# Kernel tuning notes

Hardware: AMD Instinct MI355X
Metric: run time of the kernel (lower is better)

## Reference

```python
import jax, jax.numpy as jnp
import numpy as np

B, C, N, H = 4, 512, 2048, 8
D = C // H  # per-head depth = 64
EPS = 1e-5


def conv1x1(x, W, b):
    # x: [B, Cin, N], W: [Cout, Cin], b: [Cout]
    return jnp.einsum('oc,bcn->bon', W, x) + b[None, :, None]


def instance_norm(x):
    # normalize over length dim per (batch, channel), no affine
    mu = jnp.mean(x, axis=-1, keepdims=True)
    var = jnp.var(x, axis=-1, keepdims=True)
    return (x - mu) * jax.lax.rsqrt(var + EPS)


def _pipeline(src, tgt, Wq, bq, Wk, bk, Wv, bv, Wm, bm):
    # query from src, key/value from tgt; reshape C -> (D outer, H inner)
    q = conv1x1(src, Wq, bq).reshape(B, D, H, N)
    k = conv1x1(tgt, Wk, bk).reshape(B, D, H, N)
    v = conv1x1(tgt, Wv, bv).reshape(B, D, H, N)
    scores = jnp.einsum('bdhn,bdhm->bhnm', q, k) / jnp.sqrt(jnp.float32(D))
    probs = jax.nn.softmax(scores, axis=-1)
    out = jnp.einsum('bhnm,bdhm->bdhn', probs, v).reshape(B, C, N)
    return conv1x1(out, Wm, bm)


def _mlp(x, W1, b1, W2, b2):
    h = conv1x1(x, W1, b1)
    h = jax.nn.relu(instance_norm(h))
    return conv1x1(h, W2, b2)


def setup_inputs() -> dict:
    key = jax.random.key(0)
    ks = jax.random.split(key, 8)
    s = 0.02
    return {
        'source_features': jax.random.normal(ks[0], (B, C, N), jnp.float32),
        'target_features': jax.random.normal(ks[1], (B, C, N), jnp.float32),
        'Wq': jax.random.normal(ks[2], (C, C), jnp.float32) * s,
        'bq': jnp.zeros((C,), jnp.float32),
        'Wk': jax.random.normal(ks[3], (C, C), jnp.float32) * s,
        'bk': jnp.zeros((C,), jnp.float32),
        'Wv': jax.random.normal(ks[4], (C, C), jnp.float32) * s,
        'bv': jnp.zeros((C,), jnp.float32),
        'Wm': jax.random.normal(ks[5], (C, C), jnp.float32) * s,
        'bm': jnp.zeros((C,), jnp.float32),
        'W1': jax.random.normal(ks[6], (2 * C, 2 * C), jnp.float32) * s,
        'b1': jnp.zeros((2 * C,), jnp.float32),
        'W2': jax.random.normal(ks[7], (C, 2 * C), jnp.float32) * s,
        'b2': jnp.zeros((C,), jnp.float32),
    }


def reference(source_features, target_features, Wq, bq, Wk, bk, Wv, bv, Wm, bm, W1, b1, W2, b2):
    src, tgt = source_features, target_features
    # source update uses ORIGINAL target features
    src_att = _pipeline(src, tgt, Wq, bq, Wk, bk, Wv, bv, Wm, bm)
    src = src + _mlp(jnp.concatenate([src, src_att], axis=1), W1, b1, W2, b2)
    # target update uses the UPDATED source features (in-place semantics of original)
    tgt_att = _pipeline(tgt, src, Wq, bq, Wk, bk, Wv, bv, Wm, bm)
    tgt = tgt + _mlp(jnp.concatenate([tgt, tgt_att], axis=1), W1, b1, W2, b2)
    return src, tgt
```

## Files before the change

### kernel.cpp

```cpp
#include <hip/hip_runtime.h>

#define NN 2048
#define CC 512
#define BB 4
#define HH 8
#define DD 64
#define SCALE 0.18033688011112043f

typedef unsigned short u16;
typedef __attribute__((ext_vector_type(8))) short bf16x8;
typedef __attribute__((ext_vector_type(4))) float f32x4;

extern "C" __device__ float __ocml_native_exp2_f32(float);

__device__ inline u16 f2b(float x) {
    unsigned u = __builtin_bit_cast(unsigned, x);
    u += 0x7fffu + ((u >> 16) & 1u);
    return (u16)(u >> 16);
}
__device__ inline float b2f(u16 h) {
    unsigned u = ((unsigned)h) << 16;
    return __builtin_bit_cast(float, u);
}

#define GLD16(g, l) __builtin_amdgcn_global_load_lds( \
    (const __attribute__((address_space(1))) unsigned int*)(g), \
    (__attribute__((address_space(3))) unsigned int*)(l), 16, 0, 0)

template<int JT, bool DBUF>
__device__ __forceinline__ void gemm_core_t(
    const u16* __restrict__ Xa, const u16* __restrict__ Xb, int Ca, int K,
    const u16* __restrict__ Wt, size_t rowBase,
    u16* As, u16* Bs, f32x4 (&acc)[4][JT])
{
    constexpr int OT = JT * 32;
    constexpr int ASZ = 128 * 64, BSZ = OT * 64;
    const int tid = threadIdx.x;
    const int lane = tid & 63, w = tid >> 6;
    const int quad = lane >> 4, l16 = lane & 15;
    const int wrow = w & 1, wcol = w >> 1;
    const int arow = lane >> 3, aseg = lane & 7;
    const int asw = aseg ^ arow;
    const int lk = l16 & 7;

    auto stage = [&](int k0, u16* Ad, u16* Bd) {
        const u16* Xs; int Crow, cc;
        if (k0 < Ca) { Xs = Xa; Crow = Ca; cc = k0; }
        else         { Xs = Xb; Crow = K - Ca; cc = k0 - Ca; }
#pragma unroll
        for (int i = 0; i < 4; ++i) {
            int rl = w * 32 + i * 8 + arow;
            int la = __builtin_amdgcn_readfirstlane((w * 32 + i * 8) * 64);
            GLD16(Xs + (rowBase + rl) * (size_t)Crow + cc + asw * 8, (char*)Ad + (size_t)la * 2);
        }
#pragma unroll
        for (int i = 0; i < OT / 32; ++i) {
            int rl = w * (OT / 4) + i * 8 + arow;
            int la = __builtin_amdgcn_readfirstlane((w * (OT / 4) + i * 8) * 64);
            GLD16(Wt + (size_t)rl * K + k0 + asw * 8, (char*)Bd + (size_t)la * 2);
        }
    };
    auto compute = [&](const u16* Ac, const u16* Bc) {
#pragma unroll
        for (int kk = 0; kk < 2; ++kk) {
            const int g = ((kk * 4 + quad) ^ lk) * 8;
            bf16x8 av[4], bv[JT];
#pragma unroll
            for (int i = 0; i < 4; ++i)
                av[i] = *(const bf16x8*)&Ac[(wrow * 64 + i * 16 + l16) * 64 + g];
#pragma unroll
            for (int jj = 0; jj < JT; ++jj)
                bv[jj] = *(const bf16x8*)&Bc[(wcol * JT * 16 + jj * 16 + l16) * 64 + g];
#pragma unroll
            for (int i = 0; i < 4; ++i)
#pragma unroll
                for (int jj = 0; jj < JT; ++jj)
                    acc[i][jj] = __builtin_amdgcn_mfma_f32_16x16x32_bf16(av[i], bv[jj], acc[i][jj], 0, 0, 0);
        }
    };

    if constexpr (DBUF) {
        stage(0, As, Bs);
        const int nt = K / 64;
        for (int t = 0; t < nt; ++t) {
            const u16* Ac = As + (t & 1) * ASZ;
            const u16* Bc = Bs + (t & 1) * BSZ;
            __syncthreads();
            if (t + 1 < nt)
                stage((t + 1) * 64, As + ((t + 1) & 1) * ASZ, Bs + ((t + 1) & 1) * BSZ);
            compute(Ac, Bc);
        }
    } else {
        for (int k0 = 0; k0 < K; k0 += 64) {
            stage(k0, As, Bs);
            __syncthreads();
            compute(As, Bs);
            __syncthreads();
        }
    }
}

template<int JT>
__device__ __forceinline__ void gemm_epilogue_t(
    f32x4 (&acc)[4][JT], const float* __restrict__ bias, int mode,
    int b, int n0, int o0, int Cout,
    const float* __restrict__ res, float* __restrict__ outF, u16* __restrict__ outB)
{
    const int tid = threadIdx.x;
    const int lane = tid & 63, w = tid >> 6;
    const int quad = lane >> 4, l16 = lane & 15;
    const int wrow = w & 1, wcol = w >> 1;
    const size_t bN = (size_t)b * NN;
    const int nb0 = n0 + wrow * 64, ob0 = o0 + wcol * JT * 16;

    if (mode == 0) {
#pragma unroll
        for (int j = 0; j < JT; ++j) {
            int o = ob0 + j * 16 + l16;
            float bs = bias[o];
#pragma unroll
            for (int i = 0; i < 4; ++i)
#pragma unroll
                for (int r = 0; r < 4; ++r) {
                    int n = nb0 + i * 16 + quad * 4 + r;
                    outB[(bN + n) * Cout + o] = f2b(acc[i][j][r] + bs);
                }
        }
    } else if (mode == 1) {
#pragma unroll
        for (int j = 0; j < JT; ++j) {
            int o = ob0 + j * 16 + l16;
            float bs = bias[o];
            int h = o >> 6, d = o & 63;
#pragma unroll
            for (int i = 0; i < 4; ++i) {
                int n = nb0 + i * 16 + quad * 4;
                ushort4 pk;
                pk.x = f2b(acc[i][j][0] + bs); pk.y = f2b(acc[i][j][1] + bs);
                pk.z = f2b(acc[i][j][2] + bs); pk.w = f2b(acc[i][j][3] + bs);
                *(ushort4*)&outB[(((size_t)b * HH + h) * DD + d) * NN + n] = pk;
            }
        }
    } else {
#pragma unroll
        for (int j = 0; j < JT; ++j) {
            int o = ob0 + j * 16 + l16;
            float bs = bias[o];
#pragma unroll
            for (int i = 0; i < 4; ++i) {
                int n = nb0 + i * 16 + quad * 4;
                size_t ad = ((size_t)b * Cout + o) * NN + n;
                float4 rv = *(const float4*)&res[ad];
                float4 yv;
                yv.x = acc[i][j][0] + bs + rv.x;
                yv.y = acc[i][j][1] + bs + rv.y;
                yv.z = acc[i][j][2] + bs + rv.z;
                yv.w = acc[i][j][3] + bs + rv.w;
                *(float4*)&outF[ad] = yv;
                if (mode == 2) {
                    outB[(bN + n + 0) * Cout + o] = f2b(yv.x);
                    outB[(bN + n + 1) * Cout + o] = f2b(yv.y);
                    outB[(bN + n + 2) * Cout + o] = f2b(yv.z);
                    outB[(bN + n + 3) * Cout + o] = f2b(yv.w);
                }
            }
        }
    }
}

template<int JT>
__global__ __launch_bounds__(256, 3) void gemm_bf16_t(
    const u16* __restrict__ Wb, const float* __restrict__ bias,
    const u16* __restrict__ Xa, const u16* __restrict__ Xb,
    int Ca, int K, int Cout,
    const float* __restrict__ res, float* __restrict__ outF,
    u16* __restrict__ outB, int mode)
{
    __shared__ u16 As[2 * 128 * 64];
    __shared__ u16 Bs[2 * JT * 32 * 64];
    const int b = blockIdx.z, n0 = blockIdx.x * 128, o0 = blockIdx.y * (JT * 32);
    f32x4 acc[4][JT] = {};
    gemm_core_t<JT, true>(Xa, Xb, Ca, K, Wb + (size_t)o0 * K, (size_t)b * NN + n0, As, Bs, acc);
    gemm_epilogue_t<JT>(acc, bias, mode, b, n0, o0, Cout, res, outF, outB);
}

template<bool DBUF>
__device__ __forceinline__ void gemm_core8(
    const u16* __restrict__ Xa, const u16* __restrict__ Xb, int Ca, int K,
    const u16* __restrict__ Wt, size_t rowBase,
    u16* As, u16* Bs, f32x4 (&acc)[4][2])
{
    constexpr int ASZ = 128 * 64, BSZ = 128 * 64;
    const int tid = threadIdx.x;
    const int lane = tid & 63, w = tid >> 6;
    const int quad = lane >> 4, l16 = lane & 15;
    const int wr = w & 1, wc = w >> 1;
    const int arow = lane >> 3, aseg = lane & 7;
    const int asw = aseg ^ arow;
    const int lk = l16 & 7;

    auto stage = [&](int k0, u16* Ad, u16* Bd) {
        const u16* Xs; int Crow, cc;
        if (k0 < Ca) { Xs = Xa; Crow = Ca; cc = k0; }
        else         { Xs = Xb; Crow = K - Ca; cc = k0 - Ca; }
#pragma unroll
        for (int i = 0; i < 2; ++i) {
            int rl = w * 16 + i * 8 + arow;
            int la = __builtin_amdgcn_readfirstlane((w * 16 + i * 8) * 64);
            GLD16(Xs + (rowBase + rl) * (size_t)Crow + cc + asw * 8, (char*)Ad + (size_t)la * 2);
            GLD16(Wt + (size_t)rl * K + k0 + asw * 8, (char*)Bd + (size_t)la * 2);
        }
    };
    auto compute = [&](const u16* Ac, const u16* Bc) {
#pragma unroll
        for (int kk = 0; kk < 2; ++kk) {
            const int g = ((kk * 4 + quad) ^ lk) * 8;
            bf16x8 av[4], bv[2];
#pragma unroll
            for (int i = 0; i < 4; ++i)
                av[i] = *(const bf16x8*)&Ac[(wr * 64 + i * 16 + l16) * 64 + g];
#pragma unroll
            for (int j = 0; j < 2; ++j)
                bv[j] = *(const bf16x8*)&Bc[(wc * 32 + j * 16 + l16) * 64 + g];
#pragma unroll
            for (int i = 0; i < 4; ++i)
#pragma unroll
                for (int j = 0; j < 2; ++j)
                    acc[i][j] = __builtin_amdgcn_mfma_f32_16x16x32_bf16(av[i], bv[j], acc[i][j], 0, 0, 0);
        }
    };

    if constexpr (DBUF) {
        stage(0, As, Bs);
        const int nt = K / 64;
        for (int t = 0; t < nt; ++t) {
            const u16* Ac = As + (t & 1) * ASZ;
            const u16* Bc = Bs + (t & 1) * BSZ;
            __syncthreads();
            if (t + 1 < nt)
                stage((t + 1) * 64, As + ((t + 1) & 1) * ASZ, Bs + ((t + 1) & 1) * BSZ);
            compute(Ac, Bc);
        }
    } else {
        for (int k0 = 0; k0 < K; k0 += 64) {
            stage(k0, As, Bs);
            __syncthreads();
            compute(As, Bs);
            __syncthreads();
        }
    }
}

__device__ __forceinline__ void gemm_epilogue8(
    f32x4 (&acc)[4][2], const float* __restrict__ bias, int mode,
    int b, int n0, int o0, int Cout, u16* __restrict__ outB)
{
    const int tid = threadIdx.x;
    const int lane = tid & 63, w = tid >> 6;
    const int quad = lane >> 4, l16 = lane & 15;
    const int wr = w & 1, wc = w >> 1;
    const size_t bN = (size_t)b * NN;
    const int nb0 = n0 + wr * 64, ob0 = o0 + wc * 32;

    if (mode == 0) {
#pragma unroll
        for (int j = 0; j < 2; ++j) {
            int o = ob0 + j * 16 + l16;
            float bs = bias[o];
#pragma unroll
            for (int i = 0; i < 4; ++i)
#pragma unroll
                for (int r = 0; r < 4; ++r) {
                    int n = nb0 + i * 16 + quad * 4 + r;
                    outB[(bN + n) * Cout + o] = f2b(acc[i][j][r] + bs);
                }
        }
    } else {
#pragma unroll
        for (int j = 0; j < 2; ++j) {
            int o = ob0 + j * 16 + l16;
            float bs = bias[o];
            int h = o >> 6, d = o & 63;
#pragma unroll
            for (int i = 0; i < 4; ++i) {
                int n = nb0 + i * 16 + quad * 4;
                ushort4 pk;
                pk.x = f2b(acc[i][j][0] + bs); pk.y = f2b(acc[i][j][1] + bs);
                pk.z = f2b(acc[i][j][2] + bs); pk.w = f2b(acc[i][j][3] + bs);
                *(ushort4*)&outB[(((size_t)b * HH + h) * DD + d) * NN + n] = pk;
            }
        }
    }
}

__global__ __launch_bounds__(512, 4) void gemm_qkv(
    const u16* __restrict__ WQ, const float* __restrict__ bQ,
    const u16* __restrict__ XQ, u16* __restrict__ outQ,
    const u16* __restrict__ WK, const float* __restrict__ bK, u16* __restrict__ outK,
    const u16* __restrict__ WV, const float* __restrict__ bV, u16* __restrict__ outV,
    const u16* __restrict__ XKV)
{
    __shared__ u16 As[2 * 128 * 64];
    __shared__ u16 Bs[2 * 128 * 64];
    const int yb = blockIdx.y;
    const u16* W; const float* bias; const u16* X; u16* outB; int mode, o0;
    if (yb < 4)      { o0 = yb * 128;       W = WQ; bias = bQ; X = XQ;  outB = outQ; mode = 0; }
    else if (yb < 8) { o0 = (yb - 4) * 128; W = WK; bias = bK; X = XKV; outB = outK; mode = 0; }
    else             { o0 = (yb - 8) * 128; W = WV; bias = bV; X = XKV; outB = outV; mode = 1; }
    const int b = blockIdx.z, n0 = blockIdx.x * 128;
    f32x4 acc[4][2] = {};
    gemm_core8<true>(X, nullptr, 512, 512, W + (size_t)o0 * 512, (size_t)b * NN + n0, As, Bs, acc);
    gemm_epilogue8(acc, bias, mode, b, n0, o0, 512, outB);
}

__global__ __launch_bounds__(512, 4) void gemm_w1(
    const u16* __restrict__ Wb, const float* __restrict__ bias,
    const u16* __restrict__ Xa, const u16* __restrict__ Xb,
    u16* __restrict__ outB, float* __restrict__ Ssum, float* __restrict__ Ssq)
{
    __shared__ u16 As[2 * 128 * 64];
    __shared__ u16 Bs[2 * 128 * 64];
    const int b = blockIdx.z, n0 = blockIdx.x * 128, o0 = blockIdx.y * 128;
    f32x4 acc[4][2] = {};
    gemm_core8<true>(Xa, Xb, 512, 1024, Wb + (size_t)o0 * 1024, (size_t)b * NN + n0, As, Bs, acc);

    const int tid = threadIdx.x;
    const int lane = tid & 63, w = tid >> 6;
    const int quad = lane >> 4, l16 = lane & 15;
    const int wr = w & 1, wc = w >> 1;
    const size_t bN = (size_t)b * NN;
    const int nb0 = n0 + wr * 64, ob0 = o0 + wc * 32;

#pragma unroll
    for (int j = 0; j < 2; ++j) {
        int o = ob0 + j * 16 + l16;
        float bs = bias[o];
        float s = 0.f, q = 0.f;
#pragma unroll
        for (int i = 0; i < 4; ++i)
#pragma unroll
            for (int r = 0; r < 4; ++r) {
                int n = nb0 + i * 16 + quad * 4 + r;
                float y = acc[i][j][r] + bs;
                s += y; q += y * y;
                outB[(bN + n) * 1024 + o] = f2b(y);
            }
        s += __shfl_xor(s, 16); s += __shfl_xor(s, 32);
        q += __shfl_xor(q, 16); q += __shfl_xor(q, 32);
        if (quad == 0) {
            atomicAdd(&Ssum[b * 1024 + o], s);
            atomicAdd(&Ssq[b * 1024 + o], q);
        }
    }
}

__global__ __launch_bounds__(512, 4) void attn(
    const u16* __restrict__ Qg, const u16* __restrict__ Kg,
    const u16* __restrict__ Vg, u16* __restrict__ Og)
{
    __shared__ __align__(16) u16 pool[6 * 4096];
    u16* const Ksb[2] = { pool, pool + 4096 };
    u16* const Vtb[2] = { pool + 2 * 4096, pool + 3 * 4096 };
    u16* const Ps = pool + 4 * 4096;
    const int tid = threadIdx.x;
    const int lane = tid & 63, w = tid >> 6;
    const int qg = w & 3, hv = w >> 2;
    const int quad = lane >> 4, l16 = lane & 15;
    const int id = blockIdx.x;
    const int xcd = id & 7, jj = id >> 3;
    const int bh = xcd * 4 + (jj >> 4), nb = jj & 15;
    const int b = bh >> 3, h = bh & 7;
    const int n0 = nb * 128, wn0 = qg * 32;
    const int sr0 = w * 8;
    const size_t qkBase = ((size_t)b * NN) * CC + h * DD;
    const size_t vBase  = (((size_t)b * HH + h) * DD) * NN;
    const int r8 = lane >> 3, seg = lane & 7;
    const int segp = seg ^ r8;
    const int lk = l16 & 7;

    const u16* kp = Kg + qkBase + (size_t)(sr0 + r8) * CC + segp * 8;
    const u16* vp = Vg + vBase + (size_t)(sr0 + r8) * NN + segp * 8;

    bf16x8 qf[2][2];
#pragma unroll
    for (int qs = 0; qs < 2; ++qs) {
        int n = n0 + wn0 + qs * 16 + l16;
#pragma unroll
        for (int ks = 0; ks < 2; ++ks)
            qf[qs][ks] = *(const bf16x8*)&Qg[qkBase + (size_t)n * CC + ks * 32 + quad * 8];
    }

    const short oneb = 0x3F80;
    const bf16x8 ones = {oneb, oneb, oneb, oneb, oneb, oneb, oneb, oneb};
    f32x4 oa[2][4] = {};
    f32x4 lacc[2] = {};

    GLD16(kp, Ksb[0] + sr0 * 64);
    GLD16(vp, Vtb[0] + sr0 * 64);
    kp += 64 * CC; vp += 64;

#define ATTN_PREF(BUF) do { \
        GLD16(kp, Ksb[BUF] + sr0 * 64); \
        GLD16(vp, Vtb[BUF] + sr0 * 64); \
        kp += 64 * CC; vp += 64; \
    } while (0)

#define ATTN_BODY(CUR) do { \
        const u16* ksb = Ksb[CUR]; \
        const u16* vtb = Vtb[CUR]; \
        f32x4 st[2][2] = {}; \
        _Pragma("unroll") \
        for (int ks = 0; ks < 2; ++ks) { \
            bf16x8 ak[2]; \
            _Pragma("unroll") \
            for (int rtl = 0; rtl < 2; ++rtl) \
                ak[rtl] = *(const bf16x8*)&ksb[(hv * 32 + rtl * 16 + l16) * 64 + ((ks * 4 + quad) ^ lk) * 8]; \
            __builtin_amdgcn_s_setprio(1); \
            _Pragma("unroll") \
            for (int rtl = 0; rtl < 2; ++rtl) \
                _Pragma("unroll") \
                for (int qs = 0; qs < 2; ++qs) \
                    st[qs][rtl] = __builtin_amdgcn_mfma_f32_16x16x32_bf16(ak[rtl], qf[qs][ks], st[qs][rtl], 0, 0, 0); \
            __builtin_amdgcn_s_setprio(0); \
        } \
        _Pragma("unroll") \
        for (int qs = 0; qs < 2; ++qs) { \
            int nrow = wn0 + qs * 16 + l16; \
            _Pragma("unroll") \
            for (int rtl = 0; rtl < 2; ++rtl) { \
                unsigned u0 = __builtin_bit_cast(unsigned, __ocml_native_exp2_f32(st[qs][rtl][0])); \
                unsigned u1 = __builtin_bit_cast(unsigned, __ocml_native_exp2_f32(st[qs][rtl][1])); \
                unsigned u2 = __builtin_bit_cast(unsigned, __ocml_native_exp2_f32(st[qs][rtl][2])); \
                unsigned u3 = __builtin_bit_cast(unsigned, __ocml_native_exp2_f32(st[qs][rtl][3])); \
                uint2 t; \
                t.x = __builtin_amdgcn_perm(u1, u0, 0x07060302u); \
                t.y = __builtin_amdgcn_perm(u3, u2, 0x07060302u); \
                int g = (((hv * 2 + rtl) * 2 + (quad >> 1))) ^ lk; \
                *(uint2*)&Ps[nrow * 64 + g * 8 + (quad & 1) * 4] = t; \
            } \
        } \
        { \
            bf16x8 pa[2]; \
            _Pragma("unroll") \
            for (int qs = 0; qs < 2; ++qs) \
                pa[qs] = *(const bf16x8*)&Ps[(wn0 + qs * 16 + l16) * 64 + ((hv * 4 + quad) ^ lk) * 8]; \
            bf16x8 vb[4]; \
            _Pragma("unroll") \
            for (int ct = 0; ct < 4; ++ct) \
                vb[ct] = *(const bf16x8*)&vtb[(ct * 16 + l16) * 64 + ((hv * 4 + quad) ^ lk) * 8]; \
            __builtin_amdgcn_s_setprio(1); \
            _Pragma("unroll") \
            for (int ct = 0; ct < 4; ++ct) \
                _Pragma("unroll") \
                for (int qs = 0; qs < 2; ++qs) \
                    oa[qs][ct] = __builtin_amdgcn_mfma_f32_16x16x32_bf16(pa[qs], vb[ct], oa[qs][ct], 0, 0, 0); \
            _Pragma("unroll") \
            for (int qs = 0; qs < 2; ++qs) \
                lacc[qs] = __builtin_amdgcn_mfma_f32_16x16x32_bf16(pa[qs], ones, lacc[qs], 0, 0, 0); \
            __builtin_amdgcn_s_setprio(0); \
        } \
    } while (0)

    for (int it = 0; it < NN / 64; it += 2) {
        __syncthreads();
        ATTN_PREF(1);
        ATTN_BODY(0);
        __syncthreads();
        if (it < NN / 64 - 2)
            ATTN_PREF(0);
        ATTN_BODY(1);
    }
#undef ATTN_PREF
#undef ATTN_BODY

    __syncthreads();
    float* M = (float*)pool;
    const int mbase = (qg * 64 + lane) * 44;
    if (hv == 1) {
#pragma unroll
        for (int qs = 0; qs < 2; ++qs)
#pragma unroll
            for (int ct = 0; ct < 4; ++ct)
                *(f32x4*)&M[mbase + (qs * 4 + ct) * 4] = oa[qs][ct];
        *(f32x4*)&M[mbase + 32] = lacc[0];
        *(f32x4*)&M[mbase + 36] = lacc[1];
    }
    __syncthreads();
    if (hv == 0) {
#pragma unroll
        for (int qs = 0; qs < 2; ++qs)
#pragma unroll
            for (int ct = 0; ct < 4; ++ct)
                oa[qs][ct] += *(const f32x4*)&M[mbase + (qs * 4 + ct) * 4];
        lacc[0] += *(const f32x4*)&M[mbase + 32];
        lacc[1] += *(const f32x4*)&M[mbase + 36];
#pragma unroll
        for (int qs = 0; qs < 2; ++qs)
#pragma unroll
            for (int r = 0; r < 4; ++r) {
                float li = 1.f / lacc[qs][r];
                int n = n0 + wn0 + qs * 16 + quad * 4 + r;
#pragma unroll
                for (int ct = 0; ct < 4; ++ct)
                    Og[qkBase + (size_t)n * CC + ct * 16 + l16] = f2b(oa[qs][ct][r] * li);
            }
    }
}

__global__ __launch_bounds__(256) void transpose_cvt(
    const float* __restrict__ X, u16* __restrict__ Y)
{
    __shared__ float T[64][65];
    const int tid = threadIdx.x;
    const int n0 = blockIdx.x * 64, c0 = blockIdx.y * 64, b = blockIdx.z;
    const int rr = tid >> 4, cc4 = tid & 15;
#pragma unroll
    for (int p = 0; p < 4; ++p) {
        int cl = p * 16 + rr;
        float4 v = *(const float4*)&X[((size_t)b * CC + c0 + cl) * NN + n0 + cc4 * 4];
        T[cl][cc4 * 4 + 0] = v.x; T[cl][cc4 * 4 + 1] = v.y;
        T[cl][cc4 * 4 + 2] = v.z; T[cl][cc4 * 4 + 3] = v.w;
    }
    __syncthreads();
#pragma unroll
    for (int p = 0; p < 4; ++p) {
        int nl = p * 16 + rr;
        ushort4 pk;
        pk.x = f2b(T[cc4 * 4 + 0][nl]);
        pk.y = f2b(T[cc4 * 4 + 1][nl]);
        pk.z = f2b(T[cc4 * 4 + 2][nl]);
        pk.w = f2b(T[cc4 * 4 + 3][nl]);
        *(ushort4*)&Y[((size_t)b * NN + n0 + nl) * CC + c0 + cc4 * 4] = pk;
    }
}

__global__ __launch_bounds__(256) void prep_weights(
    const float* __restrict__ Wq, const float* __restrict__ Wk,
    const float* __restrict__ Wv, const float* __restrict__ Wm,
    const float* __restrict__ W1, const float* __restrict__ W2,
    u16* oQ, u16* oK, u16* oV, u16* oM, u16* o1, u16* o2)
{
    const float* W; u16* o; int rows, cols, perm; float sc = 1.f;
    switch (blockIdx.z) {
        case 0: W = Wq; o = oQ; rows = 512;  cols = 512;  perm = 1; sc = SCALE; break;
        case 1: W = Wk; o = oK; rows = 512;  cols = 512;  perm = 1; break;
        case 2: W = Wv; o = oV; rows = 512;  cols = 512;  perm = 1; break;
        case 3: W = Wm; o = oM; rows = 512;  cols = 512;  perm = 2; break;
        case 4: W = W1; o = o1; rows = 1024; cols = 1024; perm = 0; break;
        default: W = W2; o = o2; rows = 512; cols = 1024; perm = 0; break;
    }
    int c = blockIdx.x * 256 + threadIdx.x;
    int r = blockIdx.y;
    if (r >= rows || c >= cols) return;
    int sr = r, scol = c;
    if (perm == 1) sr = (r & 63) * 8 + (r >> 6);
    else if (perm == 2) scol = (c & 63) * 8 + (c >> 6);
    o[(size_t)r * cols + c] = f2b(W[(size_t)sr * cols + scol] * sc);
}

__global__ void prep_bias(const float* __restrict__ bq, const float* __restrict__ bk,
                          const float* __restrict__ bv,
                          float* oq, float* ok, float* ov)
{
    int i = blockIdx.x * 256 + threadIdx.x;
    int y = blockIdx.y;
    const float* s = (y == 0) ? bq : (y == 1) ? bk : bv;
    float* o = (y == 0) ? oq : (y == 1) ? ok : ov;
    float v = s[(i & 63) * 8 + (i >> 6)];
    if (y == 0) v *= SCALE;
    o[i] = v;
}

__global__ __launch_bounds__(256) void inorm_p2(
    u16* __restrict__ X, const float* __restrict__ Ssum, const float* __restrict__ Ssq)
{
    const int tid = threadIdx.x;
    const int cidx = (tid & 127) * 8;
    const int rq = tid >> 7;
    const int b = blockIdx.y, nz = blockIdx.x;
    float4 s0 = *(const float4*)&Ssum[b * 1024 + cidx];
    float4 s1 = *(const float4*)&Ssum[b * 1024 + cidx + 4];
    float4 q0 = *(const float4*)&Ssq[b * 1024 + cidx];
    float4 q1 = *(const float4*)&Ssq[b * 1024 + cidx + 4];
    float mean[8] = { s0.x, s0.y, s0.z, s0.w, s1.x, s1.y, s1.z, s1.w };
    float sq[8]   = { q0.x, q0.y, q0.z, q0.w, q1.x, q1.y, q1.z, q1.w };
    float rstd[8];
#pragma unroll
    for (int j = 0; j < 8; ++j) {
        float m = mean[j] * (1.f / NN);
        float v = sq[j] * (1.f / NN) - m * m;
        mean[j] = m; rstd[j] = rsqrtf(fmaxf(v, 0.f) + 1e-5f);
    }
    size_t base = ((size_t)b * NN + nz * 16 + rq * 8) * 1024 + cidx;
    for (int i = 0; i < 8; ++i) {
        bf16x8 v = *(const bf16x8*)&X[base + (size_t)i * 1024];
        bf16x8 o;
#pragma unroll
        for (int j = 0; j < 8; ++j) {
            float x = b2f((u16)v[j]);
            x = (x - mean[j]) * rstd[j];
            o[j] = (short)f2b(fmaxf(x, 0.f));
        }
        *(bf16x8*)&X[base + (size_t)i * 1024] = o;
    }
}

extern "C" void kernel_launch(void* const* d_in, const int* in_sizes, int n_in,
                              void* d_out, int out_size, void* d_ws, size_t ws_size,
                              hipStream_t stream)
{
    (void)in_sizes; (void)n_in; (void)out_size; (void)ws_size;
    const float* src = (const float*)d_in[0];
    const float* tgt = (const float*)d_in[1];
    const float* Wq = (const float*)d_in[2];  const float* bq = (const float*)d_in[3];
    const float* Wk = (const float*)d_in[4];  const float* bk = (const float*)d_in[5];
    const float* Wv = (const float*)d_in[6];  const float* bv = (const float*)d_in[7];
    const float* Wm = (const float*)d_in[8];  const float* bm = (const float*)d_in[9];
    const float* W1 = (const float*)d_in[10]; const float* b1 = (const float*)d_in[11];
    const float* W2 = (const float*)d_in[12]; const float* b2 = (const float*)d_in[13];

    char* w = (char*)d_ws;
    u16* WQp = (u16*)(w);
    u16* WKp = (u16*)(w + (512u << 10));
    u16* WVp = (u16*)(w + (1u << 20));
    u16* WMp = (u16*)(w + (3u << 19));
    u16* W1b = (u16*)(w + (2u << 20));
    u16* W2b = (u16*)(w + (4u << 20));
    float* BQp = (float*)(w + (5u << 20));
    float* BKp = BQp + 512;
    float* BVp = BQp + 1024;
    float* STS = BQp + 1536;
    float* STQ = STS + 4096;
    u16* X0 = (u16*)(w + ( 6u << 20));
    u16* X1 = (u16*)(w + (14u << 20));
    u16* B0 = (u16*)(w + (22u << 20));
    u16* B1 = (u16*)(w + (30u << 20));
    u16* B2 = (u16*)(w + (38u << 20));
    u16* B3 = (u16*)(w + (46u << 20));

    float* out = (float*)d_out;
    const size_t R = (size_t)BB * CC * NN;
    dim3 blk(256), blkA(512);

    prep_weights<<<dim3(4, 1024, 6), blk, 0, stream>>>(Wq, Wk, Wv, Wm, W1, W2,
                                                       WQp, WKp, WVp, WMp, W1b, W2b);
    prep_bias<<<dim3(2, 3), blk, 0, stream>>>(bq, bk, bv, BQp, BKp, BVp);
    transpose_cvt<<<dim3(32, 8, 4), blk, 0, stream>>>(src, X0);
    transpose_cvt<<<dim3(32, 8, 4), blk, 0, stream>>>(tgt, X1);

    dim3 gQKV(16, 12, 4), gM(16, 8, 4), gW1(16, 8, 4), gW2(16, 8, 4), gIN(128, 4);

    gemm_qkv<<<gQKV, blkA, 0, stream>>>(WQp, BQp, X0, B0, WKp, BKp, B1, WVp, BVp, B2, X1);
    attn<<<dim3(512), blkA, 0, stream>>>(B0, B1, B2, B3);
    gemm_bf16_t<2><<<gM, blk, 0, stream>>>(WMp, bm, B3, nullptr, 512, 512, 512, nullptr, nullptr, B0, 0);
    hipMemsetAsync(STS, 0, 8192 * sizeof(float), stream);
    gemm_w1<<<gW1, blkA, 0, stream>>>(W1b, b1, X0, B0, B1, STS, STQ);
    inorm_p2<<<gIN, blk, 0, stream>>>(B1, STS, STQ);
    gemm_bf16_t<2><<<gW2, blk, 0, stream>>>(W2b, b2, B1, nullptr, 1024, 1024, 512, src, out, B3, 2);

    gemm_qkv<<<gQKV, blkA, 0, stream>>>(WQp, BQp, X1, X0, WKp, BKp, B0, WVp, BVp, B1, B3);
    attn<<<dim3(512), blkA, 0, stream>>>(X0, B0, B1, B2);
    gemm_bf16_t<2><<<gM, blk, 0, stream>>>(WMp, bm, B2, nullptr, 512, 512, 512, nullptr, nullptr, X0, 0);
    hipMemsetAsync(STS, 0, 8192 * sizeof(float), stream);
    gemm_w1<<<gW1, blkA, 0, stream>>>(W1b, b1, X1, X0, B0, STS, STQ);
    inorm_p2<<<gIN, blk, 0, stream>>>(B0, STS, STQ);
    gemm_bf16_t<2><<<gW2, blk, 0, stream>>>(W2b, b2, B0, nullptr, 1024, 1024, 512, tgt, out + R, nullptr, 3);
}
```

Baseline: 384.5 us.

## Keep attention probabilities in registers, split keys across waves, use 16x16x16 MFMA for PV

The attention kernel is restructured so each 256-thread block handles 64 queries. Each of its 4 waves takes a 16-key slice of every 64-key tile. The exp'd score fragments are packed straight into bf16x4 registers and fed to a 16x16x16 bf16 MFMA for P·V. This removes the LDS round-trip for P and the extra MFMA against a ones vector that computed row sums, which are now accumulated as scalar sums. In exchange, the four waves' partial outputs must be tree-reduced through LDS with extra barriers at the end, and each block reloads K/V for fewer queries, which doubles K/V traffic.

```diff
diff --git a/kernel.cpp b/kernel.cpp
--- a/kernel.cpp
+++ b/kernel.cpp
@@ -9,9 +9,21 @@
 
 typedef unsigned short u16;
 typedef __attribute__((ext_vector_type(8))) short bf16x8;
+typedef __attribute__((ext_vector_type(4))) short bf16x4;
 typedef __attribute__((ext_vector_type(4))) float f32x4;
 
 extern "C" __device__ float __ocml_native_exp2_f32(float);
+
+#if __has_builtin(__builtin_amdgcn_mfma_f32_16x16x16bf16_1k)
+#define MFMA16(A, B, C) __builtin_amdgcn_mfma_f32_16x16x16bf16_1k(A, B, C, 0, 0, 0)
+#else
+__device__ __forceinline__ f32x4 mfma16_asm(bf16x4 a, bf16x4 b, f32x4 c) {
+    f32x4 d;
+    asm("v_mfma_f32_16x16x16_bf16 %0, %1, %2, %3" : "=v"(d) : "v"(a), "v"(b), "0"(c));
+    return d;
+}
+#define MFMA16(A, B, C) mfma16_asm(A, B, C)
+#endif
 
 __device__ inline u16 f2b(float x) {
     unsigned u = __builtin_bit_cast(unsigned, x);
@@ -354,111 +366,101 @@
     }
 }
 
-__global__ __launch_bounds__(512, 4) void attn(
+__global__ __launch_bounds__(256, 3) void attn(
     const u16* __restrict__ Qg, const u16* __restrict__ Kg,
     const u16* __restrict__ Vg, u16* __restrict__ Og)
 {
-    __shared__ __align__(16) u16 pool[6 * 4096];
+    __shared__ __align__(16) u16 pool[17664];
     u16* const Ksb[2] = { pool, pool + 4096 };
     u16* const Vtb[2] = { pool + 2 * 4096, pool + 3 * 4096 };
-    u16* const Ps = pool + 4 * 4096;
     const int tid = threadIdx.x;
-    const int lane = tid & 63, w = tid >> 6;
-    const int qg = w & 3, hv = w >> 2;
+    const int lane = tid & 63, hv = tid >> 6;
     const int quad = lane >> 4, l16 = lane & 15;
     const int id = blockIdx.x;
     const int xcd = id & 7, jj = id >> 3;
-    const int bh = xcd * 4 + (jj >> 4), nb = jj & 15;
+    const int bh = xcd * 4 + (jj >> 5), nb = jj & 31;
     const int b = bh >> 3, h = bh & 7;
-    const int n0 = nb * 128, wn0 = qg * 32;
-    const int sr0 = w * 8;
+    const int n0 = nb * 64;
+    const int sr0 = hv * 16;
     const size_t qkBase = ((size_t)b * NN) * CC + h * DD;
     const size_t vBase  = (((size_t)b * HH + h) * DD) * NN;
     const int r8 = lane >> 3, seg = lane & 7;
     const int segp = seg ^ r8;
     const int lk = l16 & 7;
 
-    const u16* kp = Kg + qkBase + (size_t)(sr0 + r8) * CC + segp * 8;
-    const u16* vp = Vg + vBase + (size_t)(sr0 + r8) * NN + segp * 8;
-
-    bf16x8 qf[2][2];
-#pragma unroll
-    for (int qs = 0; qs < 2; ++qs) {
-        int n = n0 + wn0 + qs * 16 + l16;
+    const u16* kp0 = Kg + qkBase + (size_t)(sr0 + r8) * CC + segp * 8;
+    const u16* kp1 = kp0 + (size_t)8 * CC;
+    const u16* vp0 = Vg + vBase + (size_t)(sr0 + r8) * NN + segp * 8;
+    const u16* vp1 = vp0 + (size_t)8 * NN;
+
+    bf16x8 qf[4][2];
+#pragma unroll
+    for (int qs = 0; qs < 4; ++qs) {
+        int n = n0 + qs * 16 + l16;
 #pragma unroll
         for (int ks = 0; ks < 2; ++ks)
             qf[qs][ks] = *(const bf16x8*)&Qg[qkBase + (size_t)n * CC + ks * 32 + quad * 8];
     }
 
-    const short oneb = 0x3F80;
-    const bf16x8 ones = {oneb, oneb, oneb, oneb, oneb, oneb, oneb, oneb};
-    f32x4 oa[2][4] = {};
-    f32x4 lacc[2] = {};
-
-    GLD16(kp, Ksb[0] + sr0 * 64);
-    GLD16(vp, Vtb[0] + sr0 * 64);
-    kp += 64 * CC; vp += 64;
+    f32x4 oa[4][4] = {};
+    float lp[4] = {};
+
+    GLD16(kp0, Ksb[0] + sr0 * 64);
+    GLD16(kp1, Ksb[0] + (sr0 + 8) * 64);
+    GLD16(vp0, Vtb[0] + sr0 * 64);
+    GLD16(vp1, Vtb[0] + (sr0 + 8) * 64);
+    kp0 += 64 * CC; kp1 += 64 * CC; vp0 += 64; vp1 += 64;
 
 #define ATTN_PREF(BUF) do { \
-        GLD16(kp, Ksb[BUF] + sr0 * 64); \
-        GLD16(vp, Vtb[BUF] + sr0 * 64); \
-        kp += 64 * CC; vp += 64; \
+        GLD16(kp0, Ksb[BUF] + sr0 * 64); \
+        GLD16(kp1, Ksb[BUF] + (sr0 + 8) * 64); \
+        GLD16(vp0, Vtb[BUF] + sr0 * 64); \
+        GLD16(vp1, Vtb[BUF] + (sr0 + 8) * 64); \
+        kp0 += 64 * CC; kp1 += 64 * CC; vp0 += 64; vp1 += 64; \
     } while (0)
 
 #define ATTN_BODY(CUR) do { \
         const u16* ksb = Ksb[CUR]; \
         const u16* vtb = Vtb[CUR]; \
-        f32x4 st[2][2] = {}; \
+         \
+        bf16x8 ak[2]; \
         _Pragma("unroll") \
-        for (int ks = 0; ks < 2; ++ks) { \
-            bf16x8 ak[2]; \
+        for (int ks = 0; ks < 2; ++ks) \
+            ak[ks] = *(const bf16x8*)&ksb[(sr0 + l16) * 64 + ((ks * 4 + quad) ^ lk) * 8]; \
+         \
+        bf16x4 vb[4]; \
+        _Pragma("unroll") \
+        for (int ct = 0; ct < 4; ++ct) { \
+            int g = (hv * 2 + (quad >> 1)) ^ lk; \
+            vb[ct] = *(const bf16x4*)&vtb[(ct * 16 + l16) * 64 + g * 8 + (quad & 1) * 4]; \
+        } \
+         \
+        bf16x4 pa[4]; \
+        _Pragma("unroll") \
+        for (int qs = 0; qs < 4; ++qs) { \
+            f32x4 st = {}; \
+            __builtin_amdgcn_s_setprio(1); \
+            st = __builtin_amdgcn_mfma_f32_16x16x32_bf16(ak[0], qf[qs][0], st, 0, 0, 0); \
+            st = __builtin_amdgcn_mfma_f32_16x16x32_bf16(ak[1], qf[qs][1], st, 0, 0, 0); \
+            __builtin_amdgcn_s_setprio(0); \
+            float e0 = __ocml_native_exp2_f32(st[0]); \
+            float e1 = __ocml_native_exp2_f32(st[1]); \
+            float e2 = __ocml_native_exp2_f32(st[2]); \
+            float e3 = __ocml_native_exp2_f32(st[3]); \
+            lp[qs] += (e0 + e1) + (e2 + e3); \
+            uint2 t; \
+            t.x = __builtin_amdgcn_perm(__builtin_bit_cast(unsigned, e1), __builtin_bit_cast(unsigned, e0), 0x07060302u); \
+            t.y = __builtin_amdgcn_perm(__builtin_bit_cast(unsigned, e3), __builtin_bit_cast(unsigned, e2), 0x07060302u); \
+            pa[qs] = __builtin_bit_cast(bf16x4, t); \
+        } \
+         \
+        __builtin_amdgcn_s_setprio(1); \
+        _Pragma("unroll") \
+        for (int ct = 0; ct < 4; ++ct) \
             _Pragma("unroll") \
-            for (int rtl = 0; rtl < 2; ++rtl) \
-                ak[rtl] = *(const bf16x8*)&ksb[(hv * 32 + rtl * 16 + l16) * 64 + ((ks * 4 + quad) ^ lk) * 8]; \
-            __builtin_amdgcn_s_setprio(1); \
-            _Pragma("unroll") \
-            for (int rtl = 0; rtl < 2; ++rtl) \
-                _Pragma("unroll") \
-                for (int qs = 0; qs < 2; ++qs) \
-                    st[qs][rtl] = __builtin_amdgcn_mfma_f32_16x16x32_bf16(ak[rtl], qf[qs][ks], st[qs][rtl], 0, 0, 0); \
-            __builtin_amdgcn_s_setprio(0); \
-        } \
-        _Pragma("unroll") \
-        for (int qs = 0; qs < 2; ++qs) { \
-            int nrow = wn0 + qs * 16 + l16; \
-            _Pragma("unroll") \
-            for (int rtl = 0; rtl < 2; ++rtl) { \
-                unsigned u0 = __builtin_bit_cast(unsigned, __ocml_native_exp2_f32(st[qs][rtl][0])); \
-                unsigned u1 = __builtin_bit_cast(unsigned, __ocml_native_exp2_f32(st[qs][rtl][1])); \
-                unsigned u2 = __builtin_bit_cast(unsigned, __ocml_native_exp2_f32(st[qs][rtl][2])); \
-                unsigned u3 = __builtin_bit_cast(unsigned, __ocml_native_exp2_f32(st[qs][rtl][3])); \
-                uint2 t; \
-                t.x = __builtin_amdgcn_perm(u1, u0, 0x07060302u); \
-                t.y = __builtin_amdgcn_perm(u3, u2, 0x07060302u); \
-                int g = (((hv * 2 + rtl) * 2 + (quad >> 1))) ^ lk; \
-                *(uint2*)&Ps[nrow * 64 + g * 8 + (quad & 1) * 4] = t; \
-            } \
-        } \
-        { \
-            bf16x8 pa[2]; \
-            _Pragma("unroll") \
-            for (int qs = 0; qs < 2; ++qs) \
-                pa[qs] = *(const bf16x8*)&Ps[(wn0 + qs * 16 + l16) * 64 + ((hv * 4 + quad) ^ lk) * 8]; \
-            bf16x8 vb[4]; \
-            _Pragma("unroll") \
-            for (int ct = 0; ct < 4; ++ct) \
-                vb[ct] = *(const bf16x8*)&vtb[(ct * 16 + l16) * 64 + ((hv * 4 + quad) ^ lk) * 8]; \
-            __builtin_amdgcn_s_setprio(1); \
-            _Pragma("unroll") \
-            for (int ct = 0; ct < 4; ++ct) \
-                _Pragma("unroll") \
-                for (int qs = 0; qs < 2; ++qs) \
-                    oa[qs][ct] = __builtin_amdgcn_mfma_f32_16x16x32_bf16(pa[qs], vb[ct], oa[qs][ct], 0, 0, 0); \
-            _Pragma("unroll") \
-            for (int qs = 0; qs < 2; ++qs) \
-                lacc[qs] = __builtin_amdgcn_mfma_f32_16x16x32_bf16(pa[qs], ones, lacc[qs], 0, 0, 0); \
-            __builtin_amdgcn_s_setprio(0); \
-        } \
+            for (int qs = 0; qs < 4; ++qs) \
+                oa[qs][ct] = MFMA16(pa[qs], vb[ct], oa[qs][ct]); \
+        __builtin_amdgcn_s_setprio(0); \
     } while (0)
 
     for (int it = 0; it < NN / 64; it += 2) {
@@ -475,35 +477,72 @@
 
     __syncthreads();
     float* M = (float*)pool;
-    const int mbase = (qg * 64 + lane) * 44;
-    if (hv == 1) {
-#pragma unroll
-        for (int qs = 0; qs < 2; ++qs)
+    float* SA = M;
+    float* SB = M + 64 * 68;
+    float* lbuf = M + 2 * 64 * 68;
+    const int mb = lane * 68;
+
+    if (hv == 1 || hv == 3) {
+        float* S = (hv == 1) ? SA : SB;
+#pragma unroll
+        for (int qs = 0; qs < 4; ++qs)
 #pragma unroll
             for (int ct = 0; ct < 4; ++ct)
-                *(f32x4*)&M[mbase + (qs * 4 + ct) * 4] = oa[qs][ct];
-        *(f32x4*)&M[mbase + 32] = lacc[0];
-        *(f32x4*)&M[mbase + 36] = lacc[1];
+                *(f32x4*)&S[mb + (qs * 4 + ct) * 4] = oa[qs][ct];
+#pragma unroll
+        for (int qs = 0; qs < 4; ++qs) S[mb + 64 + qs] = lp[qs];
     }
     __syncthreads();
     if (hv == 0) {
 #pragma unroll
-        for (int qs = 0; qs < 2; ++qs)
+        for (int qs = 0; qs < 4; ++qs) {
 #pragma unroll
             for (int ct = 0; ct < 4; ++ct)
-                oa[qs][ct] += *(const f32x4*)&M[mbase + (qs * 4 + ct) * 4];
-        lacc[0] += *(const f32x4*)&M[mbase + 32];
-        lacc[1] += *(const f32x4*)&M[mbase + 36];
-#pragma unroll
-        for (int qs = 0; qs < 2; ++qs)
+                oa[qs][ct] += *(const f32x4*)&SA[mb + (qs * 4 + ct) * 4];
+            lp[qs] += SA[mb + 64 + qs];
+        }
+    } else if (hv == 2) {
+#pragma unroll
+        for (int qs = 0; qs < 4; ++qs) {
+#pragma unroll
+            for (int ct = 0; ct < 4; ++ct)
+                oa[qs][ct] += *(const f32x4*)&SB[mb + (qs * 4 + ct) * 4];
+            lp[qs] += SB[mb + 64 + qs];
+        }
+    }
+    __syncthreads();
+    if (hv == 2) {
+#pragma unroll
+        for (int qs = 0; qs < 4; ++qs) {
+#pragma unroll
+            for (int ct = 0; ct < 4; ++ct)
+                *(f32x4*)&SA[mb + (qs * 4 + ct) * 4] = oa[qs][ct];
+            SA[mb + 64 + qs] = lp[qs];
+        }
+    }
+    __syncthreads();
+    if (hv == 0) {
+#pragma unroll
+        for (int qs = 0; qs < 4; ++qs) {
+#pragma unroll
+            for (int ct = 0; ct < 4; ++ct)
+                oa[qs][ct] += *(const f32x4*)&SA[mb + (qs * 4 + ct) * 4];
+            lp[qs] += SA[mb + 64 + qs];
+            float l = lp[qs];
+            l += __shfl_xor(l, 16); l += __shfl_xor(l, 32);
+            if (quad == 0) lbuf[qs * 16 + l16] = l;
+        }
+#pragma unroll
+        for (int qs = 0; qs < 4; ++qs) {
 #pragma unroll
             for (int r = 0; r < 4; ++r) {
-                float li = 1.f / lacc[qs][r];
-                int n = n0 + wn0 + qs * 16 + quad * 4 + r;
+                float li = 1.f / lbuf[qs * 16 + quad * 4 + r];
+                int n = n0 + qs * 16 + quad * 4 + r;
 #pragma unroll
                 for (int ct = 0; ct < 4; ++ct)
                     Og[qkBase + (size_t)n * CC + ct * 16 + l16] = f2b(oa[qs][ct][r] * li);
             }
+        }
     }
 }
 
@@ -651,7 +690,7 @@
     dim3 gQKV(16, 12, 4), gM(16, 8, 4), gW1(16, 8, 4), gW2(16, 8, 4), gIN(128, 4);
 
     gemm_qkv<<<gQKV, blkA, 0, stream>>>(WQp, BQp, X0, B0, WKp, BKp, B1, WVp, BVp, B2, X1);
-    attn<<<dim3(512), blkA, 0, stream>>>(B0, B1, B2, B3);
+    attn<<<dim3(1024), blk, 0, stream>>>(B0, B1, B2, B3);
     gemm_bf16_t<2><<<gM, blk, 0, stream>>>(WMp, bm, B3, nullptr, 512, 512, 512, nullptr, nullptr, B0, 0);
     hipMemsetAsync(STS, 0, 8192 * sizeof(float), stream);
     gemm_w1<<<gW1, blkA, 0, stream>>>(W1b, b1, X0, B0, B1, STS, STQ);
@@ -659,7 +698,7 @@
     gemm_bf16_t<2><<<gW2, blk, 0, stream>>>(W2b, b2, B1, nullptr, 1024, 1024, 512, src, out, B3, 2);
 
     gemm_qkv<<<gQKV, blkA, 0, stream>>>(WQp, BQp, X1, X0, WKp, BKp, B0, WVp, BVp, B1, B3);
-    attn<<<dim3(512), blkA, 0, stream>>>(X0, B0, B1, B2);
+    attn<<<dim3(1024), blk, 0, stream>>>(X0, B0, B1, B2);
     gemm_bf16_t<2><<<gM, blk, 0, stream>>>(WMp, bm, B2, nullptr, 512, 512, 512, nullptr, nullptr, X0, 0);
     hipMemsetAsync(STS, 0, 8192 * sizeof(float), stream);
     gemm_w1<<<gW1, blkA, 0, stream>>>(W1b, b1, X1, X0, B0, STS, STQ);
```

New measurement: 408.1 us. 1.06x slower.
